# Kernel tuning notes

Measured on AMD Instinct MI355X. Metric: run time of the kernel, lower is better.

The kernel has to match this reference:

```python
import jax, jax.numpy as jnp
import numpy as np
from jax.scipy.stats import norm

B, T = 64, 1024
RNN_DIM, EMB_DIM, ATTN_DIM = 1024, 512, 128
N_FILT, KSIZE, N_MEAN = 32, 31, 8
LOGVAR_MIN = float(np.log(0.1 ** 2))
LOGVAR_MAX = float(np.log(36.77 ** 2))


def setup_inputs() -> dict:
    key = jax.random.key(0)
    ks = jax.random.split(key, 10)
    return {
        "attention_hidden_state": jax.random.normal(ks[0], (B, RNN_DIM), jnp.float32),
        "memory": jax.random.normal(ks[1], (B, T, EMB_DIM), jnp.float32),
        "processed_memory": jax.random.normal(ks[2], (B, T, ATTN_DIM), jnp.float32),
        "attention_weights_cat": jax.random.uniform(ks[3], (B, 2, T), jnp.float32),
        "prev_means": jnp.zeros((B,), jnp.float32),
        "mask": jnp.zeros((B, T), bool),
        # learned parameters (all Linear layers bias=False; conv bias=False)
        "W_query": jax.random.normal(ks[4], (ATTN_DIM, RNN_DIM), jnp.float32) * 0.02,
        "conv_w": jax.random.normal(ks[5], (N_FILT, 2, KSIZE), jnp.float32) * 0.1,
        "W_loc": jax.random.normal(ks[6], (ATTN_DIM, N_FILT), jnp.float32) * 0.1,
        "W_mean": jax.random.normal(ks[7], (N_MEAN, ATTN_DIM), jnp.float32) * 0.05,
        "W_logvar": jax.random.normal(ks[8], (1, ATTN_DIM), jnp.float32) * 0.05,
    }


def reference(attention_hidden_state, memory, processed_memory, attention_weights_cat,
              prev_means, mask, W_query, conv_w, W_loc, W_mean, W_logvar):
    pad = (KSIZE - 1) // 2
    # query projection: [B, 1, attn_dim]
    processed_query = (attention_hidden_state @ W_query.T)[:, None, :]
    # location layer: conv1d(2 -> n_filters, same padding) then dense -> [B, T, attn_dim]
    loc = jax.lax.conv_general_dilated(
        attention_weights_cat, conv_w, window_strides=(1,),
        padding=[(pad, pad)], dimension_numbers=("NCH", "OIH", "NCH"))  # [B, F, T]
    processed_loc = jnp.einsum("bft,df->btd", loc, W_loc)
    pred = jnp.tanh(processed_query + processed_loc + processed_memory)  # [B, T, D]
    avg = pred.mean(axis=1)                                              # [B, D]
    # monotonic mean increment (soft_clip = softplus, keeps increments positive)
    mean_inc = jax.nn.softplus(avg @ W_mean.T).sum(axis=-1)              # [B]
    means = prev_means + mean_inc                                        # [B]
    logvars = (LOGVAR_MAX - LOGVAR_MIN) * jax.nn.sigmoid(avg @ W_logvar.T) + LOGVAR_MIN
    stds = jnp.exp(0.5 * logvars[:, 0])                                  # [B]
    # Gaussian window: CDF(x+0.5) - CDF(x-0.5), x = 0..T-1
    x = jnp.arange(T, dtype=jnp.float32)[None, :]                        # [1, T]
    mu, sd = means[:, None], stds[:, None]
    p = norm.cdf((x + 0.5 - mu) / sd) - norm.cdf((x - 0.5 - mu) / sd)    # [B, T]
    attention_weights = jnp.where(mask, 0.0, p)
    attention_context = jnp.einsum("bt,bte->be", attention_weights, memory)
    return attention_context, attention_weights
```

## Files before the change

### kernel.cpp

```cpp
#include <hip/hip_runtime.h>
#include <math.h>

#define B 64
#define T 1024
#define RNN_DIM 1024
#define EMB_DIM 512
#define ATTN_DIM 128
#define N_FILT 32
#define KSIZE 31
#define N_MEAN 8

#define LOGVAR_MIN (-4.605170185988091f)
#define LOGVAR_MAX (7.2093654f)

#define TTILE 256
#define AWWIN 288
#define MAGIC 0x73C0FFEEu
#define TWO_LOG2E 2.8853900817779268f

typedef __attribute__((ext_vector_type(8))) short bf16x8;
typedef __attribute__((ext_vector_type(4))) float f32x4;

__device__ __forceinline__ unsigned short f2bf(float x) {
    unsigned u = __float_as_uint(x);
    u += 0x7FFFu + ((u >> 16) & 1u);
    return (unsigned short)(u >> 16);
}

__device__ __forceinline__ float fast_tanh(float x) {
    float e = __builtin_amdgcn_exp2f(x * TWO_LOG2E);
    return 1.f - 2.f * __builtin_amdgcn_rcpf(e + 1.f);
}

__global__ __launch_bounds__(512, 1) void fused_kernel(
        const float* __restrict__ hidden,
        const float* __restrict__ memory,
        const float* __restrict__ pm,
        const float* __restrict__ awcat,
        const float* __restrict__ prevm,
        const unsigned char* __restrict__ mask,
        const float* __restrict__ Wq,
        const float* __restrict__ convw,
        const float* __restrict__ Wloc,
        const float* __restrict__ Wmean,
        const float* __restrict__ Wlogvar,
        unsigned* __restrict__ pqflags,
        unsigned* __restrict__ avgflags,
        float* __restrict__ pq_ws,
        float* __restrict__ avg_part,
        float* __restrict__ out_ctx,
        float* __restrict__ out_w) {
    __shared__ __align__(16) float aw_s[2][AWWIN];
    __shared__ __align__(16) float pq_s[ATTN_DIM];
    __shared__ __align__(16) unsigned short loc_bf[TTILE * 32];
    __shared__ __align__(16) unsigned short wl_bf[ATTN_DIM * 32];
    __shared__ __align__(16) float red2[8][ATTN_DIM];
    __shared__ __align__(16) float a_s[ATTN_DIM];
    __shared__ float w_s[T];
    __shared__ __align__(16) float4 cred_s[16][32];
    __shared__ float musd_s[2];
    __shared__ int slo_s[8], shi_s[8];

    const int x = blockIdx.x;
    const int b = blockIdx.y;
    const int tid = threadIdx.x;
    const int t0 = x * TTILE;
    const int lane = tid & 63;
    const int w = tid >> 6;

    for (int idx = tid; idx < 2 * AWWIN; idx += 512) {
        int c = idx / AWWIN, j = idx - c * AWWIN;
        int tg = t0 - 16 + j;
        aw_s[c][j] = (tg >= 0 && tg < T) ? awcat[(size_t)b * 2 * T + c * T + tg] : 0.f;
    }

    {
        int d = tid >> 2, seg = tid & 3;
        const float4* wsrc = (const float4*)Wloc + tid * 2;
        float4 v0 = wsrc[0], v1 = wsrc[1];
        uint4 pk;
        pk.x = (unsigned)f2bf(v0.x) | ((unsigned)f2bf(v0.y) << 16);
        pk.y = (unsigned)f2bf(v0.z) | ((unsigned)f2bf(v0.w) << 16);
        pk.z = (unsigned)f2bf(v1.x) | ((unsigned)f2bf(v1.y) << 16);
        pk.w = (unsigned)f2bf(v1.z) | ((unsigned)f2bf(v1.w) << 16);
        int prow = (d & 7) * 16 + (d >> 3);
        *(uint4*)&wl_bf[prow * 32 + seg * 8] = pk;
    }

    {
        const float4* h4 = (const float4*)(hidden + (size_t)b * RNN_DIM);
        float4 hv0 = h4[lane], hv1 = h4[lane + 64];
        float4 hv2 = h4[lane + 128], hv3 = h4[lane + 192];
#pragma unroll
        for (int pass = 0; pass < 4; ++pass) {
            int d = x * 32 + pass * 8 + w;
            const float4* w4 = (const float4*)(Wq + (size_t)d * RNN_DIM);
            float4 wa = w4[lane], wb = w4[lane + 64];
            float4 wc = w4[lane + 128], wd = w4[lane + 192];
            float acc = hv0.x * wa.x + hv0.y * wa.y + hv0.z * wa.z + hv0.w * wa.w;
            acc += hv1.x * wb.x + hv1.y * wb.y + hv1.z * wb.z + hv1.w * wb.w;
            acc += hv2.x * wc.x + hv2.y * wc.y + hv2.z * wc.z + hv2.w * wc.w;
            acc += hv3.x * wd.x + hv3.y * wd.y + hv3.z * wd.z + hv3.w * wd.w;
#pragma unroll
            for (int off = 32; off > 0; off >>= 1)
                acc += __shfl_xor(acc, off, 64);
            if (lane == 0)
                __hip_atomic_store(&pq_ws[b * ATTN_DIM + d], acc,
                                   __ATOMIC_RELAXED, __HIP_MEMORY_SCOPE_AGENT);
        }
        asm volatile("s_waitcnt vmcnt(0)" ::: "memory");
    }
    __syncthreads();
    if (tid == 0)
        __hip_atomic_store(&pqflags[b * 4 + x], MAGIC,
                           __ATOMIC_RELEASE, __HIP_MEMORY_SCOPE_AGENT);

    {
        int f = tid & 31, tg8 = tid >> 5;
        float cw0[KSIZE], cw1[KSIZE];
#pragma unroll
        for (int k = 0; k < KSIZE; ++k) {
            cw0[k] = convw[(f * 2 + 0) * KSIZE + k];
            cw1[k] = convw[(f * 2 + 1) * KSIZE + k];
        }
#pragma unroll
        for (int p = 0; p < 2; ++p) {
            int o = tg8 + 16 * p;
            float a0[40], a1[40];
#pragma unroll
            for (int j = 0; j < 10; ++j) {
                float4 v0 = *(const float4*)&aw_s[0][o * 8 + 4 * j];
                float4 v1 = *(const float4*)&aw_s[1][o * 8 + 4 * j];
                a0[4 * j] = v0.x; a0[4 * j + 1] = v0.y; a0[4 * j + 2] = v0.z; a0[4 * j + 3] = v0.w;
                a1[4 * j] = v1.x; a1[4 * j + 1] = v1.y; a1[4 * j + 2] = v1.z; a1[4 * j + 3] = v1.w;
            }
#pragma unroll
            for (int i = 0; i < 8; ++i) {
                float s = 0.f;
#pragma unroll
                for (int k = 0; k < KSIZE; ++k)
                    s += a0[i + k + 1] * cw0[k] + a1[i + k + 1] * cw1[k];
                loc_bf[(o * 8 + i) * 32 + f] = f2bf(s);
            }
        }
    }
    __syncthreads();

    {
        int col = lane & 15;
        int kg = lane >> 4;

        float pmr[2][4][8];
#pragma unroll
        for (int m = 0; m < 2; ++m)
#pragma unroll
            for (int j = 0; j < 4; ++j) {
                const float* rowp = pm
                    + (size_t)(b * T + t0 + w * 32 + m * 16 + kg * 4 + j) * ATTN_DIM
                    + col * 8;
                float4 v0 = *(const float4*)rowp;
                float4 v1 = *(const float4*)(rowp + 4);
                pmr[m][j][0] = v0.x; pmr[m][j][1] = v0.y;
                pmr[m][j][2] = v0.z; pmr[m][j][3] = v0.w;
                pmr[m][j][4] = v1.x; pmr[m][j][5] = v1.y;
                pmr[m][j][6] = v1.z; pmr[m][j][7] = v1.w;
            }

        bf16x8 bfrag[8];
#pragma unroll
        for (int n = 0; n < 8; ++n)
            bfrag[n] = *(const bf16x8*)&wl_bf[(n * 16 + col) * 32 + kg * 8];
        bf16x8 af[2];
#pragma unroll
        for (int m = 0; m < 2; ++m)
            af[m] = *(const bf16x8*)&loc_bf[(w * 32 + m * 16 + col) * 32 + kg * 8];

        if (tid == 0) {
#pragma unroll
            for (int s = 0; s < 4; ++s) {
                const unsigned* fp = &pqflags[b * 4 + s];
                while (__hip_atomic_load(fp, __ATOMIC_RELAXED, __HIP_MEMORY_SCOPE_AGENT) != MAGIC)
                    __builtin_amdgcn_s_sleep(1);
            }
        }
        __syncthreads();
        if (tid < ATTN_DIM)
            pq_s[tid] = __hip_atomic_load(&pq_ws[b * ATTN_DIM + tid],
                                          __ATOMIC_RELAXED, __HIP_MEMORY_SCOPE_AGENT);
        __syncthreads();

        float pqv[8];
#pragma unroll
        for (int n = 0; n < 8; ++n) pqv[n] = pq_s[col * 8 + n];

        float accs[8];
#pragma unroll
        for (int n = 0; n < 8; ++n) accs[n] = 0.f;
#pragma unroll
        for (int m = 0; m < 2; ++m) {
#pragma unroll
            for (int n = 0; n < 8; ++n) {
                f32x4 c = {0.f, 0.f, 0.f, 0.f};
                c = __builtin_amdgcn_mfma_f32_16x16x32_bf16(af[m], bfrag[n], c, 0, 0, 0);
#pragma unroll
                for (int j = 0; j < 4; ++j)
                    accs[n] += fast_tanh(c[j] + pqv[n] + pmr[m][j][n]);
            }
        }
#pragma unroll
        for (int n = 0; n < 8; ++n) {
            float s = accs[n];
            s += __shfl_xor(s, 16, 64);
            s += __shfl_xor(s, 32, 64);
            if (lane < 16) red2[w][lane * 8 + n] = s;
        }
    }
    __syncthreads();

    if (tid < ATTN_DIM) {
        float s = 0.f;
#pragma unroll
        for (int w2 = 0; w2 < 8; ++w2) s += red2[w2][tid];
        __hip_atomic_store(&avg_part[((size_t)b * 4 + x) * ATTN_DIM + tid], s,
                           __ATOMIC_RELAXED, __HIP_MEMORY_SCOPE_AGENT);
    }
    asm volatile("s_waitcnt vmcnt(0)" ::: "memory");
    __syncthreads();
    if (tid == 0) {
        __hip_atomic_store(&avgflags[b * 4 + x], MAGIC,
                           __ATOMIC_RELEASE, __HIP_MEMORY_SCOPE_AGENT);
#pragma unroll
        for (int s = 0; s < 4; ++s) {
            const unsigned* fp = &avgflags[b * 4 + s];
            while (__hip_atomic_load(fp, __ATOMIC_RELAXED, __HIP_MEMORY_SCOPE_AGENT) != MAGIC)
                __builtin_amdgcn_s_sleep(1);
        }
    }
    __syncthreads();

    if (tid < ATTN_DIM) {
        float s = 0.f;
#pragma unroll
        for (int ss = 0; ss < 4; ++ss)
            s += __hip_atomic_load(&avg_part[((size_t)b * 4 + ss) * ATTN_DIM + tid],
                                   __ATOMIC_RELAXED, __HIP_MEMORY_SCOPE_AGENT);
        a_s[tid] = s * (1.f / (float)T);
    }
    __syncthreads();

    if (tid < 64) {
        float macc[N_MEAN];
#pragma unroll
        for (int m = 0; m < N_MEAN; ++m) macc[m] = 0.f;
        float lv = 0.f;
#pragma unroll
        for (int i = 0; i < 2; ++i) {
            int d = tid + i * 64;
            float a = a_s[d];
#pragma unroll
            for (int m = 0; m < N_MEAN; ++m) macc[m] += a * Wmean[m * ATTN_DIM + d];
            lv += a * Wlogvar[d];
        }
#pragma unroll
        for (int off = 32; off > 0; off >>= 1) {
#pragma unroll
            for (int m = 0; m < N_MEAN; ++m) macc[m] += __shfl_xor(macc[m], off, 64);
            lv += __shfl_xor(lv, off, 64);
        }
        if (tid == 0) {
            float mean_inc = 0.f;
#pragma unroll
            for (int m = 0; m < N_MEAN; ++m) {
                float xx = macc[m];
                mean_inc += fmaxf(xx, 0.f) + log1pf(expf(-fabsf(xx)));
            }
            float mu = prevm[b] + mean_inc;
            float sig = 1.f / (1.f + expf(-lv));
            float logvar = (LOGVAR_MAX - LOGVAR_MIN) * sig + LOGVAR_MIN;
            musd_s[0] = mu;
            musd_s[1] = 1.f / expf(0.5f * logvar);
        }
    }
    __syncthreads();

    float mu = musd_s[0];
    float rsd = musd_s[1];
    const float is2 = 0.7071067811865476f;
    int lo = T, hi = -1;
#pragma unroll
    for (int r = 0; r < 2; ++r) {
        int t = tid + r * 512;
        float z1 = ((float)t + 0.5f - mu) * rsd * is2;
        float z2 = ((float)t - 0.5f - mu) * rsd * is2;
        float p = 0.5f * (erff(z1) - erff(z2));
        if (mask[(size_t)b * T + t]) p = 0.f;
        w_s[t] = p;
        if ((t >> 8) == x) out_w[(size_t)b * T + t] = p;
        if (p != 0.f) { lo = min(lo, t); hi = max(hi, t); }
    }
#pragma unroll
    for (int off = 32; off > 0; off >>= 1) {
        lo = min(lo, __shfl_xor(lo, off, 64));
        hi = max(hi, __shfl_xor(hi, off, 64));
    }
    if (lane == 0) { slo_s[w] = lo; shi_s[w] = hi; }
    __syncthreads();
#pragma unroll
    for (int wv = 0; wv < 8; ++wv) {
        lo = min(lo, slo_s[wv]);
        hi = max(hi, shi_s[wv]);
    }

    {
        int e = tid & 31;
        int e4 = x * 32 + e;
        int trow = tid >> 5;
        const float4* m4 = (const float4*)memory + (size_t)b * T * (EMB_DIM / 4);
        float4 acc = make_float4(0.f, 0.f, 0.f, 0.f);
        for (int t = lo + trow; t <= hi; t += 16) {
            float wvv = w_s[t];
            float4 mm = m4[(size_t)t * (EMB_DIM / 4) + e4];
            acc.x += wvv * mm.x;
            acc.y += wvv * mm.y;
            acc.z += wvv * mm.z;
            acc.w += wvv * mm.w;
        }
        if (trow != 0) cred_s[trow][e] = acc;
        __syncthreads();
        if (trow == 0) {
#pragma unroll
            for (int r = 1; r < 16; ++r) {
                float4 o = cred_s[r][e];
                acc.x += o.x; acc.y += o.y; acc.z += o.z; acc.w += o.w;
            }
            ((float4*)(out_ctx + (size_t)b * EMB_DIM))[e4] = acc;
        }
    }
}

extern "C" void kernel_launch(void* const* d_in, const int* in_sizes, int n_in,
                              void* d_out, int out_size, void* d_ws, size_t ws_size,
                              hipStream_t stream) {
    const float* hidden  = (const float*)d_in[0];
    const float* memory  = (const float*)d_in[1];
    const float* pm      = (const float*)d_in[2];
    const float* awcat   = (const float*)d_in[3];
    const float* prevm   = (const float*)d_in[4];
    const unsigned char* mask = (const unsigned char*)d_in[5];
    const float* Wq      = (const float*)d_in[6];
    const float* convw   = (const float*)d_in[7];
    const float* Wloc    = (const float*)d_in[8];
    const float* Wmean   = (const float*)d_in[9];
    const float* Wlogvar = (const float*)d_in[10];

    unsigned* pqflags  = (unsigned*)d_ws;
    unsigned* avgflags = pqflags + 256;
    float* pq_ws       = (float*)d_ws + 512;
    float* avg_part    = pq_ws + B * ATTN_DIM;

    float* out_ctx = (float*)d_out;
    float* out_w   = out_ctx + B * EMB_DIM;

    fused_kernel<<<dim3(4, B), 512, 0, stream>>>(
        hidden, memory, pm, awcat, prevm, mask, Wq, convw, Wloc, Wmean,
        Wlogvar, pqflags, avgflags, pq_ws, avg_part, out_ctx, out_w);
}
```

Baseline: 31.19 us.

## Swap grid axes, prefetch processed memory before conv, split conv channels

The launch grid is transposed so blockIdx.x indexes the batch and blockIdx.y the time tile, which changes the order blocks are dispatched. The processed_memory register loads move ahead of the location convolution so their global latency overlaps the conv compute. The convolution now handles one input channel at a time, holding 31 weights and 40 inputs instead of double that, to lower register pressure. The softplus sum is spread across 8 lanes and combined with shuffles instead of running serially in thread 0. The earlier pm loads keep those registers live through the conv, and the new dispatch order could matter for the inter-block spin-wait flags.

```diff
diff --git a/kernel.cpp b/kernel.cpp
--- a/kernel.cpp
+++ b/kernel.cpp
@@ -61,12 +61,14 @@
     __shared__ float musd_s[2];
     __shared__ int slo_s[8], shi_s[8];
 
-    const int x = blockIdx.x;
-    const int b = blockIdx.y;
+    const int b = blockIdx.x;
+    const int x = blockIdx.y;
     const int tid = threadIdx.x;
     const int t0 = x * TTILE;
     const int lane = tid & 63;
     const int w = tid >> 6;
+    const int col = lane & 15;
+    const int kg = lane >> 4;
 
     for (int idx = tid; idx < 2 * AWWIN; idx += 512) {
         int c = idx / AWWIN, j = idx - c * AWWIN;
@@ -75,7 +77,7 @@
     }
 
     {
-        int d = tid >> 2, seg = tid & 3;
+        int d = tid >> 2;
         const float4* wsrc = (const float4*)Wloc + tid * 2;
         float4 v0 = wsrc[0], v1 = wsrc[1];
         uint4 pk;
@@ -84,7 +86,7 @@
         pk.z = (unsigned)f2bf(v1.x) | ((unsigned)f2bf(v1.y) << 16);
         pk.w = (unsigned)f2bf(v1.z) | ((unsigned)f2bf(v1.w) << 16);
         int prow = (d & 7) * 16 + (d >> 3);
-        *(uint4*)&wl_bf[prow * 32 + seg * 8] = pk;
+        *(uint4*)&wl_bf[prow * 32 + (tid & 3) * 8] = pk;
     }
 
     {
@@ -115,57 +117,60 @@
         __hip_atomic_store(&pqflags[b * 4 + x], MAGIC,
                            __ATOMIC_RELEASE, __HIP_MEMORY_SCOPE_AGENT);
 
+    float pmr[2][4][8];
+#pragma unroll
+    for (int m = 0; m < 2; ++m)
+#pragma unroll
+        for (int j = 0; j < 4; ++j) {
+            const float* rowp = pm
+                + (size_t)(b * T + t0 + w * 32 + m * 16 + kg * 4 + j) * ATTN_DIM
+                + col * 8;
+            float4 v0 = *(const float4*)rowp;
+            float4 v1 = *(const float4*)(rowp + 4);
+            pmr[m][j][0] = v0.x; pmr[m][j][1] = v0.y;
+            pmr[m][j][2] = v0.z; pmr[m][j][3] = v0.w;
+            pmr[m][j][4] = v1.x; pmr[m][j][5] = v1.y;
+            pmr[m][j][6] = v1.z; pmr[m][j][7] = v1.w;
+        }
+
     {
         int f = tid & 31, tg8 = tid >> 5;
-        float cw0[KSIZE], cw1[KSIZE];
-#pragma unroll
-        for (int k = 0; k < KSIZE; ++k) {
-            cw0[k] = convw[(f * 2 + 0) * KSIZE + k];
-            cw1[k] = convw[(f * 2 + 1) * KSIZE + k];
-        }
 #pragma unroll
         for (int p = 0; p < 2; ++p) {
             int o = tg8 + 16 * p;
-            float a0[40], a1[40];
-#pragma unroll
-            for (int j = 0; j < 10; ++j) {
-                float4 v0 = *(const float4*)&aw_s[0][o * 8 + 4 * j];
-                float4 v1 = *(const float4*)&aw_s[1][o * 8 + 4 * j];
-                a0[4 * j] = v0.x; a0[4 * j + 1] = v0.y; a0[4 * j + 2] = v0.z; a0[4 * j + 3] = v0.w;
-                a1[4 * j] = v1.x; a1[4 * j + 1] = v1.y; a1[4 * j + 2] = v1.z; a1[4 * j + 3] = v1.w;
+            float s[8];
+#pragma unroll
+            for (int i = 0; i < 8; ++i) s[i] = 0.f;
+#pragma unroll
+            for (int c = 0; c < 2; ++c) {
+                float cw[KSIZE];
+#pragma unroll
+                for (int k = 0; k < KSIZE; ++k)
+                    cw[k] = convw[(f * 2 + c) * KSIZE + k];
+                float a[40];
+#pragma unroll
+                for (int j = 0; j < 10; ++j) {
+                    float4 v = *(const float4*)&aw_s[c][o * 8 + 4 * j];
+                    a[4 * j] = v.x; a[4 * j + 1] = v.y;
+                    a[4 * j + 2] = v.z; a[4 * j + 3] = v.w;
+                }
+#pragma unroll
+                for (int i = 0; i < 8; ++i) {
+                    float t = 0.f;
+#pragma unroll
+                    for (int k = 0; k < KSIZE; ++k)
+                        t += a[i + k + 1] * cw[k];
+                    s[i] += t;
+                }
             }
 #pragma unroll
-            for (int i = 0; i < 8; ++i) {
-                float s = 0.f;
-#pragma unroll
-                for (int k = 0; k < KSIZE; ++k)
-                    s += a0[i + k + 1] * cw0[k] + a1[i + k + 1] * cw1[k];
-                loc_bf[(o * 8 + i) * 32 + f] = f2bf(s);
-            }
-        }
-    }
-    __syncthreads();
-
-    {
-        int col = lane & 15;
-        int kg = lane >> 4;
-
-        float pmr[2][4][8];
-#pragma unroll
-        for (int m = 0; m < 2; ++m)
-#pragma unroll
-            for (int j = 0; j < 4; ++j) {
-                const float* rowp = pm
-                    + (size_t)(b * T + t0 + w * 32 + m * 16 + kg * 4 + j) * ATTN_DIM
-                    + col * 8;
-                float4 v0 = *(const float4*)rowp;
-                float4 v1 = *(const float4*)(rowp + 4);
-                pmr[m][j][0] = v0.x; pmr[m][j][1] = v0.y;
-                pmr[m][j][2] = v0.z; pmr[m][j][3] = v0.w;
-                pmr[m][j][4] = v1.x; pmr[m][j][5] = v1.y;
-                pmr[m][j][6] = v1.z; pmr[m][j][7] = v1.w;
-            }
-
+            for (int i = 0; i < 8; ++i)
+                loc_bf[(o * 8 + i) * 32 + f] = f2bf(s[i]);
+        }
+    }
+    __syncthreads();
+
+    {
         bf16x8 bfrag[8];
 #pragma unroll
         for (int n = 0; n < 8; ++n)
@@ -267,14 +272,16 @@
             for (int m = 0; m < N_MEAN; ++m) macc[m] += __shfl_xor(macc[m], off, 64);
             lv += __shfl_xor(lv, off, 64);
         }
+        float mval = (lane == 0) ? macc[0] : (lane == 1) ? macc[1]
+                   : (lane == 2) ? macc[2] : (lane == 3) ? macc[3]
+                   : (lane == 4) ? macc[4] : (lane == 5) ? macc[5]
+                   : (lane == 6) ? macc[6] : macc[7];
+        float sp = fmaxf(mval, 0.f) + log1pf(expf(-fabsf(mval)));
+        sp += __shfl_xor(sp, 1, 64);
+        sp += __shfl_xor(sp, 2, 64);
+        sp += __shfl_xor(sp, 4, 64);
         if (tid == 0) {
-            float mean_inc = 0.f;
-#pragma unroll
-            for (int m = 0; m < N_MEAN; ++m) {
-                float xx = macc[m];
-                mean_inc += fmaxf(xx, 0.f) + log1pf(expf(-fabsf(xx)));
-            }
-            float mu = prevm[b] + mean_inc;
+            float mu = prevm[b] + sp;
             float sig = 1.f / (1.f + expf(-lv));
             float logvar = (LOGVAR_MAX - LOGVAR_MIN) * sig + LOGVAR_MIN;
             musd_s[0] = mu;
@@ -361,7 +368,7 @@
     float* out_ctx = (float*)d_out;
     float* out_w   = out_ctx + B * EMB_DIM;
 
-    fused_kernel<<<dim3(4, B), 512, 0, stream>>>(
+    fused_kernel<<<dim3(B, 4), 512, 0, stream>>>(
         hidden, memory, pm, awcat, prevm, mask, Wq, convw, Wloc, Wmean,
         Wlogvar, pqflags, avgflags, pq_ws, avg_part, out_ctx, out_w);
 }
```

Result: no change. 31.30 us (+0.3%).
